# Performance work log

Hardware: AMD Instinct MI355X
Metric: run time of the kernel (lower is better)

## Reference

```python
import jax, jax.numpy as jnp
import numpy as np

B, L, D = 2, 2048, 2048
H, KVH = 16, 4
DK = D // H            # 128
REP = H // KVH         # 4
CAP = 50.0


def _rope(x):
    # x: [B, h, L, DK]; rotate-half style RoPE matching the torch module
    half = DK // 2
    inv_freq = 1.0 / (10000.0 ** (jnp.arange(0, DK, 2, dtype=jnp.float32) / DK))
    pos = jnp.arange(x.shape[2], dtype=jnp.float32)
    freqs = pos[:, None] * inv_freq[None, :]          # [L, DK/2]
    cos = jnp.cos(freqs).astype(x.dtype)
    sin = jnp.sin(freqs).astype(x.dtype)
    x1, x2 = x[..., :half], x[..., half:]
    return jnp.concatenate([x1 * cos - x2 * sin, x1 * sin + x2 * cos], axis=-1)


def setup_inputs() -> dict:
    key = jax.random.key(0)
    ks = jax.random.split(key, 7)
    query = jax.random.normal(ks[0], (B, L, D), jnp.float32)
    key_t = jax.random.normal(ks[1], (B, L, D), jnp.float32)
    value = jax.random.normal(ks[2], (B, L, D), jnp.float32)
    mask = jnp.tril(jnp.ones((L, L), dtype=bool))[None, None]  # causal, broadcast over B,H
    s = 1.0 / np.sqrt(D)
    Wq = jax.random.normal(ks[3], (D, D), jnp.float32) * s
    Wk = jax.random.normal(ks[4], (D // REP, D), jnp.float32) * s
    Wv = jax.random.normal(ks[5], (D // REP, D), jnp.float32) * s
    Wo = jax.random.normal(ks[6], (D, D), jnp.float32) * s
    return {"query": query, "key_t": key_t, "value": value, "mask": mask,
            "Wq": Wq, "Wk": Wk, "Wv": Wv, "Wo": Wo}


def reference(query, key_t, value, mask, Wq, Wk, Wv, Wo):
    Lk = key_t.shape[1]
    Q = (query @ Wq.T).reshape(B, L, H, DK).transpose(0, 2, 1, 3)        # [B,H,L,DK]
    K = (key_t @ Wk.T).reshape(B, Lk, KVH, DK).transpose(0, 2, 1, 3)     # [B,KVH,Lk,DK]
    V = (value @ Wv.T).reshape(B, Lk, KVH, DK).transpose(0, 2, 1, 3)
    # repeat_interleave KV heads to match query heads (GQA)
    K = jnp.repeat(K, REP, axis=1)
    V = jnp.repeat(V, REP, axis=1)
    Q = _rope(Q)
    K = _rope(K)
    # module implements "softcap" as a clamp on q/k pre-SDPA
    Q = jnp.clip(Q, -CAP, CAP)
    K = jnp.clip(K, -CAP, CAP)
    scale = 1.0 / np.sqrt(DK)  # SDPA default scaling
    logits = jnp.einsum('bhld,bhkd->bhlk', Q, K) * scale
    neg = jnp.finfo(logits.dtype).min
    logits = logits + jnp.where(mask, jnp.zeros((), logits.dtype), neg)
    attn = jax.nn.softmax(logits, axis=-1)
    out = jnp.einsum('bhlk,bhkd->bhld', attn, V)                         # [B,H,L,DK]
    out = out.transpose(0, 2, 1, 3).reshape(B, L, D)
    return out @ Wo.T
```

## Files before the change

kernel.cpp:

```cpp
#include <hip/hip_runtime.h>

typedef __bf16 bf16;
typedef __bf16 bf16x8 __attribute__((ext_vector_type(8)));
typedef float  f32x4  __attribute__((ext_vector_type(4)));

#define MFMA16(a, b, c) __builtin_amdgcn_mfma_f32_16x16x32_bf16((a), (b), (c), 0, 0, 0)

__device__ inline void gl_lds16(const bf16* g, bf16* l) {
  __builtin_amdgcn_global_load_lds(
      (const __attribute__((address_space(1))) void*)g,
      (__attribute__((address_space(3))) void*)l, 16, 0, 0);
}

__device__ inline bf16x8 cvt8(const float* __restrict__ f) {
  float4 a = *(const float4*)f;
  float4 b = *(const float4*)(f + 4);
  bf16x8 r;
  r[0] = (bf16)a.x; r[1] = (bf16)a.y; r[2] = (bf16)a.z; r[3] = (bf16)a.w;
  r[4] = (bf16)b.x; r[5] = (bf16)b.y; r[6] = (bf16)b.z; r[7] = (bf16)b.w;
  return r;
}

__global__ void cvt_f32_bf16(const float* __restrict__ src, bf16* __restrict__ dst,
                             int n8) {
  int i = blockIdx.x * 256 + threadIdx.x;
  if (i >= n8) return;
  *(bf16x8*)(dst + (size_t)i * 8) = cvt8(src + (size_t)i * 8);
}

template <bool AF32, bool OUTF32>
__global__ __launch_bounds__(256) void gemm_bt(const void* __restrict__ Ap0,
                                               const void* __restrict__ Ap1,
                                               const bf16* __restrict__ W,
                                               void* __restrict__ C0,
                                               void* __restrict__ C1,
                                               int Nsplit, int ld0, int ld1,
                                               int M, int N, int K) {
  __shared__ alignas(16) bf16 As[16 * 512];
  __shared__ alignas(16) bf16 Bs[16 * 512];

  const int tid  = threadIdx.x;
  const int wave = tid >> 6, lane = tid & 63;
  const int wm = wave >> 1, wn = wave & 1;
  const int lr = lane & 15, quad = lane >> 4;
  const int m0 = blockIdx.y * 128, n0 = blockIdx.x * 128;

  const bool second = (n0 >= Nsplit);
  const void* Ap = second ? Ap1 : Ap0;

  f32x4 vzero = {0.f, 0.f, 0.f, 0.f};
  f32x4 acc[4][4];
#pragma unroll
  for (int mt = 0; mt < 4; ++mt)
#pragma unroll
    for (int nt = 0; nt < 4; ++nt) acc[mt][nt] = vzero;

  for (int k0 = 0; k0 < K; k0 += 64) {
#pragma unroll
    for (int j = 0; j < 4; ++j) {
      int c = wave * 4 + j;
      gl_lds16(W + (size_t)(n0 + (c >> 1) * 16 + lr) * K + k0 + (c & 1) * 32 + quad * 8,
               Bs + c * 512);
    }
    if (AF32) {
#pragma unroll
      for (int j = 0; j < 4; ++j) {
        int c = wave * 4 + j;
        *(bf16x8*)(As + c * 512 + lane * 8) =
            cvt8((const float*)Ap + (size_t)(m0 + (c >> 1) * 16 + lr) * K +
                 k0 + (c & 1) * 32 + quad * 8);
      }
    } else {
#pragma unroll
      for (int j = 0; j < 4; ++j) {
        int c = wave * 4 + j;
        gl_lds16((const bf16*)Ap + (size_t)(m0 + (c >> 1) * 16 + lr) * K +
                     k0 + (c & 1) * 32 + quad * 8,
                 As + c * 512);
      }
    }
    __syncthreads();

#pragma unroll
    for (int s = 0; s < 2; ++s) {
      bf16x8 af[4], bfg[4];
#pragma unroll
      for (int mt = 0; mt < 4; ++mt)
        af[mt] = *(const bf16x8*)(As + ((wm * 4 + mt) * 2 + s) * 512 + lane * 8);
#pragma unroll
      for (int nt = 0; nt < 4; ++nt)
        bfg[nt] = *(const bf16x8*)(Bs + ((wn * 4 + nt) * 2 + s) * 512 + lane * 8);
#pragma unroll
      for (int mt = 0; mt < 4; ++mt)
#pragma unroll
        for (int nt = 0; nt < 4; ++nt)
          acc[mt][nt] = MFMA16(af[mt], bfg[nt], acc[mt][nt]);
    }
    __syncthreads();
  }

  void* Cb = second ? C1 : C0;
  const int ld = second ? ld1 : ld0;
  const int nb = second ? n0 - Nsplit : n0;
#pragma unroll
  for (int mt = 0; mt < 4; ++mt) {
    int row = m0 + wm * 64 + mt * 16 + quad * 4;
#pragma unroll
    for (int nt = 0; nt < 4; ++nt) {
      int col = nb + wn * 64 + nt * 16 + lr;
#pragma unroll
      for (int e = 0; e < 4; ++e) {
        if (OUTF32)
          ((float*)Cb)[(size_t)(row + e) * ld + col] = acc[mt][nt][e];
        else
          ((bf16*)Cb)[(size_t)(row + e) * ld + col] = (bf16)acc[mt][nt][e];
      }
    }
  }
}

__global__ void rope_clip(bf16* __restrict__ X, int heads, float scl) {
  int tpr = heads * 8;
  int idx = blockIdx.x * 256 + threadIdx.x;
  if (idx >= 4096 * tpr) return;
  int r = idx / tpr;
  int rem = idx - r * tpr;
  int h = rem >> 3, j0 = (rem & 7) * 8;
  int l = r & 2047;
  size_t base = (size_t)r * (heads * 128) + h * 128 + j0;
  bf16x8 x1 = *(const bf16x8*)(X + base);
  bf16x8 x2 = *(const bf16x8*)(X + base + 64);
  bf16x8 y1, y2;
#pragma unroll
  for (int t = 0; t < 8; ++t) {
    int j = j0 + t;
    float inv = expf(-(float)j * (9.210340371976184f / 64.0f));
    float s, c;
    sincosf((float)l * inv, &s, &c);
    float a = (float)x1[t], b = (float)x2[t];
    float u = a * c - b * s;
    float v = a * s + b * c;
    y1[t] = (bf16)(fminf(fmaxf(u, -50.f), 50.f) * scl);
    y2[t] = (bf16)(fminf(fmaxf(v, -50.f), 50.f) * scl);
  }
  *(bf16x8*)(X + base)      = y1;
  *(bf16x8*)(X + base + 64) = y2;
}

__global__ void transpose_bf16(const bf16* __restrict__ in, bf16* __restrict__ out,
                               int R, int Cc) {
  __shared__ bf16 t[32][33];
  int b = blockIdx.z;
  const bf16* ip = in + (size_t)b * R * Cc;
  bf16* op = out + (size_t)b * R * Cc;
  int c0 = blockIdx.x * 32, r0 = blockIdx.y * 32;
  int lx = threadIdx.x, ly = threadIdx.y;
#pragma unroll
  for (int i = 0; i < 32; i += 8)
    t[ly + i][lx] = ip[(size_t)(r0 + ly + i) * Cc + c0 + lx];
  __syncthreads();
#pragma unroll
  for (int i = 0; i < 32; i += 8)
    op[(size_t)(c0 + ly + i) * R + r0 + lx] = t[lx][ly + i];
}

__global__ __launch_bounds__(512) void flash(const bf16* __restrict__ Q,
                                             const bf16* __restrict__ Kp,
                                             const bf16* __restrict__ Vt,
                                             bf16* __restrict__ Ctx) {
  __shared__ alignas(16) bf16 Ks[16 * 512];
  __shared__ alignas(16) bf16 Vs[16 * 512];
  __shared__ alignas(16) bf16 Ps[8 * 16 * 72];

  const int tid  = threadIdx.x;
  const int wave = tid >> 6, lane = tid & 63;
  const int lr = lane & 15, quad = lane >> 4;
  const int bh = blockIdx.y;
  const int b = bh >> 4, h = bh & 15, hk = h >> 2;
  const int ix = blockIdx.x;
  const int qt = (ix & 1) ? (15 - (ix >> 1)) : (ix >> 1);
  const int q0 = qt * 128;
  const int qb = q0 + wave * 16;

  const bf16* qptr = Q + ((size_t)(b * 2048 + qb + lr)) * 2048 + h * 128 + quad * 8;
  bf16x8 qf[4];
#pragma unroll
  for (int ks = 0; ks < 4; ++ks) qf[ks] = *(const bf16x8*)(qptr + ks * 32);

  f32x4 vzero = {0.f, 0.f, 0.f, 0.f};
  f32x4 o[8];
#pragma unroll
  for (int dt = 0; dt < 8; ++dt) o[dt] = vzero;
  float fls[4] = {0.f, 0.f, 0.f, 0.f};

  const bf16* kbase = Kp + (size_t)(b * 2048) * 512 + hk * 128;
  const bf16* vbase = Vt + ((size_t)(b * 512 + hk * 128)) * 2048;

  const int kmax = q0 + 128;
  for (int k0 = 0; k0 < kmax; k0 += 64) {
#pragma unroll
    for (int j = 0; j < 4; ++j) {
      int c = wave * 4 + j;
      if (c < 16) {
        gl_lds16(kbase + (size_t)(k0 + (c >> 2) * 16 + lr) * 512 + (c & 3) * 32 + quad * 8,
                 Ks + c * 512);
      } else {
        int c2 = c - 16;
        gl_lds16(vbase + (size_t)((c2 >> 1) * 16 + lr) * 2048 + k0 + (c2 & 1) * 32 + quad * 8,
                 Vs + c2 * 512);
      }
    }
    __syncthreads();

    if (k0 <= qb + 15) {
      f32x4 s[4] = {vzero, vzero, vzero, vzero};
#pragma unroll
      for (int ks = 0; ks < 4; ++ks) {
#pragma unroll
        for (int kt = 0; kt < 4; ++kt) {
          bf16x8 kf = *(const bf16x8*)(Ks + (kt * 4 + ks) * 512 + lane * 8);
          s[kt] = MFMA16(qf[ks], kf, s[kt]);
        }
      }
      bf16* pw = Ps + wave * (16 * 72);
#pragma unroll
      for (int kt = 0; kt < 4; ++kt) {
        int kid = k0 + kt * 16 + lr;
#pragma unroll
        for (int e = 0; e < 4; ++e) {
          int qi = qb + quad * 4 + e;
          float p = (kid <= qi) ? __expf(s[kt][e]) : 0.f;
          fls[e] += p;
          pw[(quad * 4 + e) * 72 + kt * 16 + lr] = (bf16)p;
        }
      }
#pragma unroll
      for (int ks2 = 0; ks2 < 2; ++ks2) {
        bf16x8 pf = *(const bf16x8*)(pw + lr * 72 + ks2 * 32 + quad * 8);
#pragma unroll
        for (int dt = 0; dt < 8; ++dt) {
          bf16x8 vf = *(const bf16x8*)(Vs + (dt * 2 + ks2) * 512 + lane * 8);
          o[dt] = MFMA16(pf, vf, o[dt]);
        }
      }
    }
    __syncthreads();
  }

#pragma unroll
  for (int e = 0; e < 4; ++e) {
    float s = fls[e];
    s += __shfl_xor(s, 1);
    s += __shfl_xor(s, 2);
    s += __shfl_xor(s, 4);
    s += __shfl_xor(s, 8);
    fls[e] = 1.0f / s;
  }

  bf16* cptr = Ctx + ((size_t)(b * 2048 + qb + quad * 4)) * 2048 + h * 128 + lr;
#pragma unroll
  for (int dt = 0; dt < 8; ++dt)
#pragma unroll
    for (int e = 0; e < 4; ++e)
      cptr[(size_t)e * 2048 + dt * 16] = (bf16)(o[dt][e] * fls[e]);
}

extern "C" void kernel_launch(void* const* d_in, const int* in_sizes, int n_in,
                              void* d_out, int out_size, void* d_ws, size_t ws_size,
                              hipStream_t stream) {
  (void)in_sizes; (void)n_in; (void)out_size; (void)ws_size;
  const float* query = (const float*)d_in[0];
  const float* key_t = (const float*)d_in[1];
  const float* value = (const float*)d_in[2];
  const float* Wq = (const float*)d_in[4];
  const float* Wk = (const float*)d_in[5];
  const float* Wv = (const float*)d_in[6];
  const float* Wo = (const float*)d_in[7];

  const size_t MB = 1024ull * 1024ull;
  char* ws  = (char*)d_ws;
  bf16* qbf = (bf16*)(ws);
  bf16* wqb = (bf16*)(ws + 16 * MB);
  bf16* wkb = (bf16*)(ws + 24 * MB);
  bf16* wvb = (bf16*)(ws + 26 * MB);
  bf16* wob = (bf16*)(ws + 28 * MB);
  bf16* Qb  = (bf16*)(ws + 36 * MB);
  bf16* Kb  = (bf16*)(ws + 52 * MB);
  bf16* Vb  = (bf16*)(ws + 56 * MB);
  bf16* Vtb = (bf16*)(ws + 60 * MB);
  bf16* Ctx = qbf;

  cvt_f32_bf16<<<4096, 256, 0, stream>>>(query, qbf, 1048576);
  cvt_f32_bf16<<<2048, 256, 0, stream>>>(Wq, wqb, 524288);
  cvt_f32_bf16<<<512, 256, 0, stream>>>(Wk, wkb, 131072);
  cvt_f32_bf16<<<512, 256, 0, stream>>>(Wv, wvb, 131072);
  cvt_f32_bf16<<<2048, 256, 0, stream>>>(Wo, wob, 524288);

  gemm_bt<false, false><<<dim3(16, 32), 256, 0, stream>>>(
      qbf, qbf, wqb, Qb, Qb, 2048, 2048, 2048, 4096, 2048, 2048);

  gemm_bt<true, false><<<dim3(8, 32), 256, 0, stream>>>(
      key_t, value, wkb, Kb, Vb, 512, 512, 512, 4096, 1024, 2048);

  rope_clip<<<2048, 256, 0, stream>>>(Qb, 16, 0.08838834764831845f);
  rope_clip<<<512, 256, 0, stream>>>(Kb, 4, 1.0f);

  transpose_bf16<<<dim3(16, 64, 2), dim3(32, 8), 0, stream>>>(Vb, Vtb, 2048, 512);

  flash<<<dim3(16, 32), 512, 0, stream>>>(Qb, Kb, Vtb, Ctx);

  gemm_bt<false, true><<<dim3(16, 32), 256, 0, stream>>>(
      Ctx, Ctx, wob, (float*)d_out, (float*)d_out, 2048, 2048, 2048, 4096, 2048, 2048);
}
```

Before: 484.2 us.

## Pair causal query tiles per block and double-buffer K/V loads in flash

Each flash block now handles two query tiles, p and 15-p, so every block does the same amount of causal work. Each K/V tile staged into LDS is reused by both Q tiles. K/V staging is double-buffered with explicit vmcnt waits so the next tile's global-to-LDS load overlaps compute on the current one. The cost is half as many blocks (256), twice the accumulator registers under a 2-wave-per-SIMD launch bound, and doubled LDS, which may hurt occupancy or cause spills.

```diff
diff --git a/kernel.cpp b/kernel.cpp
--- a/kernel.cpp
+++ b/kernel.cpp
@@ -164,105 +164,183 @@
     op[(size_t)(c0 + ly + i) * R + r0 + lx] = t[lx][ly + i];
 }
 
-__global__ __launch_bounds__(512) void flash(const bf16* __restrict__ Q,
-                                             const bf16* __restrict__ Kp,
-                                             const bf16* __restrict__ Vt,
-                                             bf16* __restrict__ Ctx) {
-  __shared__ alignas(16) bf16 Ks[16 * 512];
-  __shared__ alignas(16) bf16 Vs[16 * 512];
-  __shared__ alignas(16) bf16 Ps[8 * 16 * 72];
+__global__ __launch_bounds__(512, 2) void flash(const bf16* __restrict__ Q,
+                                                const bf16* __restrict__ Kp,
+                                                const bf16* __restrict__ Vt,
+                                                bf16* __restrict__ Ctx) {
+  __shared__ alignas(16) bf16 Ks[2][16 * 512];
+  __shared__ alignas(16) bf16 Vs[2][16 * 512];
+  __shared__ alignas(16) bf16 Ps[8][32 * 72];
 
   const int tid  = threadIdx.x;
   const int wave = tid >> 6, lane = tid & 63;
   const int lr = lane & 15, quad = lane >> 4;
   const int bh = blockIdx.y;
   const int b = bh >> 4, h = bh & 15, hk = h >> 2;
-  const int ix = blockIdx.x;
-  const int qt = (ix & 1) ? (15 - (ix >> 1)) : (ix >> 1);
-  const int q0 = qt * 128;
-  const int qb = q0 + wave * 16;
-
-  const bf16* qptr = Q + ((size_t)(b * 2048 + qb + lr)) * 2048 + h * 128 + quad * 8;
-  bf16x8 qf[4];
-#pragma unroll
-  for (int ks = 0; ks < 4; ++ks) qf[ks] = *(const bf16x8*)(qptr + ks * 32);
+  const int p = blockIdx.x;
+  const int qA0 = p * 128, qB0 = (15 - p) * 128;
+  const int qbA = qA0 + wave * 16;
+  const int qbB = qB0 + wave * 16;
+  const int nt = (qB0 + 128) >> 6;
+
+  bf16x8 qfA[4], qfB[4];
+  {
+    const bf16* qa = Q + ((size_t)(b * 2048 + qbA + lr)) * 2048 + h * 128 + quad * 8;
+    const bf16* qbp = Q + ((size_t)(b * 2048 + qbB + lr)) * 2048 + h * 128 + quad * 8;
+#pragma unroll
+    for (int ks = 0; ks < 4; ++ks) {
+      qfA[ks] = *(const bf16x8*)(qa + ks * 32);
+      qfB[ks] = *(const bf16x8*)(qbp + ks * 32);
+    }
+  }
 
   f32x4 vzero = {0.f, 0.f, 0.f, 0.f};
-  f32x4 o[8];
-#pragma unroll
-  for (int dt = 0; dt < 8; ++dt) o[dt] = vzero;
-  float fls[4] = {0.f, 0.f, 0.f, 0.f};
+  f32x4 oA[8], oB[8];
+#pragma unroll
+  for (int dt = 0; dt < 8; ++dt) { oA[dt] = vzero; oB[dt] = vzero; }
+  float flsA[4] = {0.f, 0.f, 0.f, 0.f};
+  float flsB[4] = {0.f, 0.f, 0.f, 0.f};
 
   const bf16* kbase = Kp + (size_t)(b * 2048) * 512 + hk * 128;
   const bf16* vbase = Vt + ((size_t)(b * 512 + hk * 128)) * 2048;
 
-  const int kmax = q0 + 128;
-  for (int k0 = 0; k0 < kmax; k0 += 64) {
-#pragma unroll
-    for (int j = 0; j < 4; ++j) {
-      int c = wave * 4 + j;
-      if (c < 16) {
-        gl_lds16(kbase + (size_t)(k0 + (c >> 2) * 16 + lr) * 512 + (c & 3) * 32 + quad * 8,
-                 Ks + c * 512);
-      } else {
-        int c2 = c - 16;
-        gl_lds16(vbase + (size_t)((c2 >> 1) * 16 + lr) * 2048 + k0 + (c2 & 1) * 32 + quad * 8,
-                 Vs + c2 * 512);
-      }
-    }
-    __syncthreads();
-
-    if (k0 <= qb + 15) {
-      f32x4 s[4] = {vzero, vzero, vzero, vzero};
+#define STAGE(bufi, kk)                                                         \
+  do {                                                                          \
+    _Pragma("unroll") for (int j = 0; j < 4; ++j) {                             \
+      int c = wave * 4 + j;                                                     \
+      if (c < 16) {                                                             \
+        gl_lds16(kbase + (size_t)((kk) + (c >> 2) * 16 + lr) * 512 +            \
+                     (c & 3) * 32 + quad * 8,                                   \
+                 &Ks[bufi][c * 512]);                                           \
+      } else {                                                                  \
+        int c2 = c - 16;                                                        \
+        gl_lds16(vbase + (size_t)((c2 >> 1) * 16 + lr) * 2048 + (kk) +          \
+                     (c2 & 1) * 32 + quad * 8,                                  \
+                 &Vs[bufi][c2 * 512]);                                          \
+      }                                                                         \
+    }                                                                           \
+  } while (0)
+
+  STAGE(0, 0);
+  int cur = 0;
+
+  for (int t = 0; t < nt; ++t) {
+    const int k0 = t * 64;
+    if (t + 1 < nt) {
+      STAGE(cur ^ 1, k0 + 64);
+      asm volatile("s_waitcnt vmcnt(4)" ::: "memory");
+    } else {
+      asm volatile("s_waitcnt vmcnt(0)" ::: "memory");
+    }
+    __builtin_amdgcn_s_barrier();
+
+    const bf16* ksb = Ks[cur];
+    const bf16* vsb = Vs[cur];
+
+    if (k0 <= qbA + 15) {
+      f32x4 sA[4], sB[4];
+#pragma unroll
+      for (int kt = 0; kt < 4; ++kt) { sA[kt] = vzero; sB[kt] = vzero; }
 #pragma unroll
       for (int ks = 0; ks < 4; ++ks) {
 #pragma unroll
         for (int kt = 0; kt < 4; ++kt) {
-          bf16x8 kf = *(const bf16x8*)(Ks + (kt * 4 + ks) * 512 + lane * 8);
-          s[kt] = MFMA16(qf[ks], kf, s[kt]);
-        }
-      }
-      bf16* pw = Ps + wave * (16 * 72);
+          bf16x8 kf = *(const bf16x8*)(ksb + (kt * 4 + ks) * 512 + lane * 8);
+          sA[kt] = MFMA16(qfA[ks], kf, sA[kt]);
+          sB[kt] = MFMA16(qfB[ks], kf, sB[kt]);
+        }
+      }
+      bf16* pwA = Ps[wave];
+      bf16* pwB = Ps[wave] + 16 * 72;
 #pragma unroll
       for (int kt = 0; kt < 4; ++kt) {
         int kid = k0 + kt * 16 + lr;
 #pragma unroll
         for (int e = 0; e < 4; ++e) {
-          int qi = qb + quad * 4 + e;
-          float p = (kid <= qi) ? __expf(s[kt][e]) : 0.f;
-          fls[e] += p;
-          pw[(quad * 4 + e) * 72 + kt * 16 + lr] = (bf16)p;
+          int qr = quad * 4 + e;
+          float pa = (kid <= qbA + qr) ? __expf(sA[kt][e]) : 0.f;
+          float pb = __expf(sB[kt][e]);
+          flsA[e] += pa;
+          flsB[e] += pb;
+          pwA[qr * 72 + kt * 16 + lr] = (bf16)pa;
+          pwB[qr * 72 + kt * 16 + lr] = (bf16)pb;
         }
       }
 #pragma unroll
       for (int ks2 = 0; ks2 < 2; ++ks2) {
-        bf16x8 pf = *(const bf16x8*)(pw + lr * 72 + ks2 * 32 + quad * 8);
+        bf16x8 pfA = *(const bf16x8*)(pwA + (size_t)lr * 72 + ks2 * 32 + quad * 8);
+        bf16x8 pfB = *(const bf16x8*)(pwB + (size_t)lr * 72 + ks2 * 32 + quad * 8);
 #pragma unroll
         for (int dt = 0; dt < 8; ++dt) {
-          bf16x8 vf = *(const bf16x8*)(Vs + (dt * 2 + ks2) * 512 + lane * 8);
-          o[dt] = MFMA16(pf, vf, o[dt]);
-        }
-      }
-    }
-    __syncthreads();
-  }
+          bf16x8 vf = *(const bf16x8*)(vsb + (dt * 2 + ks2) * 512 + lane * 8);
+          oA[dt] = MFMA16(pfA, vf, oA[dt]);
+          oB[dt] = MFMA16(pfB, vf, oB[dt]);
+        }
+      }
+    } else if (k0 <= qbB + 15) {
+      f32x4 s[4];
+#pragma unroll
+      for (int kt = 0; kt < 4; ++kt) s[kt] = vzero;
+#pragma unroll
+      for (int ks = 0; ks < 4; ++ks) {
+#pragma unroll
+        for (int kt = 0; kt < 4; ++kt) {
+          bf16x8 kf = *(const bf16x8*)(ksb + (kt * 4 + ks) * 512 + lane * 8);
+          s[kt] = MFMA16(qfB[ks], kf, s[kt]);
+        }
+      }
+      bf16* pwB = Ps[wave] + 16 * 72;
+#pragma unroll
+      for (int kt = 0; kt < 4; ++kt) {
+        int kid = k0 + kt * 16 + lr;
+#pragma unroll
+        for (int e = 0; e < 4; ++e) {
+          int qr = quad * 4 + e;
+          float pb = (kid <= qbB + qr) ? __expf(s[kt][e]) : 0.f;
+          flsB[e] += pb;
+          pwB[qr * 72 + kt * 16 + lr] = (bf16)pb;
+        }
+      }
+#pragma unroll
+      for (int ks2 = 0; ks2 < 2; ++ks2) {
+        bf16x8 pf = *(const bf16x8*)(pwB + (size_t)lr * 72 + ks2 * 32 + quad * 8);
+#pragma unroll
+        for (int dt = 0; dt < 8; ++dt) {
+          bf16x8 vf = *(const bf16x8*)(vsb + (dt * 2 + ks2) * 512 + lane * 8);
+          oB[dt] = MFMA16(pf, vf, oB[dt]);
+        }
+      }
+    }
+    __builtin_amdgcn_s_barrier();
+    cur ^= 1;
+  }
+#undef STAGE
 
 #pragma unroll
   for (int e = 0; e < 4; ++e) {
-    float s = fls[e];
-    s += __shfl_xor(s, 1);
-    s += __shfl_xor(s, 2);
-    s += __shfl_xor(s, 4);
-    s += __shfl_xor(s, 8);
-    fls[e] = 1.0f / s;
-  }
-
-  bf16* cptr = Ctx + ((size_t)(b * 2048 + qb + quad * 4)) * 2048 + h * 128 + lr;
+    float sa = flsA[e];
+    sa += __shfl_xor(sa, 1);
+    sa += __shfl_xor(sa, 2);
+    sa += __shfl_xor(sa, 4);
+    sa += __shfl_xor(sa, 8);
+    flsA[e] = 1.0f / sa;
+    float sb = flsB[e];
+    sb += __shfl_xor(sb, 1);
+    sb += __shfl_xor(sb, 2);
+    sb += __shfl_xor(sb, 4);
+    sb += __shfl_xor(sb, 8);
+    flsB[e] = 1.0f / sb;
+  }
+
+  bf16* ca = Ctx + ((size_t)(b * 2048 + qbA + quad * 4)) * 2048 + h * 128 + lr;
+  bf16* cb = Ctx + ((size_t)(b * 2048 + qbB + quad * 4)) * 2048 + h * 128 + lr;
 #pragma unroll
   for (int dt = 0; dt < 8; ++dt)
 #pragma unroll
-    for (int e = 0; e < 4; ++e)
-      cptr[(size_t)e * 2048 + dt * 16] = (bf16)(o[dt][e] * fls[e]);
+    for (int e = 0; e < 4; ++e) {
+      ca[(size_t)e * 2048 + dt * 16] = (bf16)(oA[dt][e] * flsA[e]);
+      cb[(size_t)e * 2048 + dt * 16] = (bf16)(oB[dt][e] * flsB[e]);
+    }
 }
 
 extern "C" void kernel_launch(void* const* d_in, const int* in_sizes, int n_in,
@@ -307,7 +385,7 @@
 
   transpose_bf16<<<dim3(16, 64, 2), dim3(32, 8), 0, stream>>>(Vb, Vtb, 2048, 512);
 
-  flash<<<dim3(16, 32), 512, 0, stream>>>(Qb, Kb, Vtb, Ctx);
+  flash<<<dim3(8, 32), 512, 0, stream>>>(Qb, Kb, Vtb, Ctx);
 
   gemm_bt<false, true><<<dim3(16, 32), 256, 0, stream>>>(
       Ctx, Ctx, wob, (float*)d_out, (float*)d_out, 2048, 2048, 2048, 4096, 2048, 2048);
```

New measurement: 460.3 us. -4.9%, faster.
